# Optimization experiments

Measured on AMD Instinct MI355X. Metric: run time of the kernel, lower is better.

The kernel has to match this reference:

```python
import jax, jax.numpy as jnp
import numpy as np

N = 400000   # nodes; must equal E because the original code computes `out + x` with out per-edge
E = 400000   # edges
HID = 128
HEADS = 4
NEG_SLOPE = 0.01  # torch F.leaky_relu default


def setup_inputs() -> dict:
    key = jax.random.key(0)
    k1, k2, k3, k4 = jax.random.split(key, 4)
    x = jax.random.normal(k1, (N, HID), dtype=jnp.float32)
    edge_index = jax.random.randint(k2, (2, E), 0, N, dtype=jnp.int64)
    # xavier-uniform-ish scale for the attention parameter [1, heads, 2*hidden]
    lim_a = float(np.sqrt(6.0 / (1 + HEADS * 2 * HID)))
    attention = jax.random.uniform(k3, (1, HEADS, 2 * HID), jnp.float32, -lim_a, lim_a)
    lim_w = float(np.sqrt(1.0 / (HID * HEADS)))
    W = jax.random.uniform(k4, (HID, HID * HEADS), jnp.float32, -lim_w, lim_w)
    b = jnp.zeros((HID,), jnp.float32)
    return {"x": x, "edge_index": edge_index, "attention": attention, "W": W, "b": b}


def _scatter_softmax(s, seg, num_segments):
    # softmax over edges grouped by destination node index `seg` (axis 0)
    m = jax.lax.stop_gradient(jax.ops.segment_max(s, seg, num_segments=num_segments))
    ex = jnp.exp(s - m[seg])
    denom = jax.ops.segment_sum(ex, seg, num_segments=num_segments)
    return ex / denom[seg]


def reference(x, edge_index, attention, W, b):
    row, col = edge_index[0], edge_index[1]
    # [E, 2*HID] per-edge concatenated features
    ef = jnp.concatenate([x[row], x[col]], axis=-1)
    # per-head scores: (ef[:,None,:] * attention).sum(-1) -> [E, HEADS]
    scores = jnp.einsum('ef,hf->eh', ef, attention[0])
    scores = jax.nn.leaky_relu(scores, NEG_SLOPE)
    scores = jax.nn.softmax(scores, axis=1)      # softmax across heads (as in source)
    # dropout(p=0.1) -> identity in eval mode
    alpha = _scatter_softmax(scores, row, N)     # [E, HEADS] per-destination softmax
    # per-head weighted source features, concatenated over heads -> [E, HEADS*HID]
    feats = (alpha[:, :, None] * x[col][:, None, :]).reshape(E, HEADS * HID)
    out = feats @ W.T + b                        # Linear(hidden*heads -> hidden)
    return out + x
```

## Files before the change

kernel.cpp:

```cpp
#include <hip/hip_runtime.h>

#define NN 400000
#define NE 400000

typedef __attribute__((ext_vector_type(4))) float f32x4;
typedef __attribute__((ext_vector_type(8))) short s16x8;
typedef unsigned short ushort_t;

__device__ __forceinline__ ushort_t f2bf(float f) {
    union { float f; unsigned int u; } c;
    c.f = f;
    unsigned int u = c.u;
    u = u + 0x7fffu + ((u >> 16) & 1u);
    return (ushort_t)(u >> 16);
}
__device__ __forceinline__ float bf2f(ushort_t v) {
    union { unsigned int u; float f; } c;
    c.u = ((unsigned int)v) << 16;
    return c.f;
}

__global__ void k_detect(const int* __restrict__ ei_raw, int* __restrict__ flag) {
    if (threadIdx.x == 0 && blockIdx.x == 0) {
        int is64 = 1;
        for (int i = 0; i < 64; i++)
            if (ei_raw[2 * i + 1] != 0) { is64 = 0; break; }
        flag[0] = is64;
    }
}

__global__ void k_cvt_idx(const int* __restrict__ ei_raw, const int* __restrict__ flag,
                          int* __restrict__ ei32) {
    const int i = blockIdx.x * 256 + threadIdx.x;
    const int f = flag[0];
    ei32[i] = f ? ei_raw[2 * i] : ei_raw[i];
}

__global__ void k_wcvt(const float* __restrict__ W, ushort_t* __restrict__ wbf) {
    const int i = blockIdx.x * 256 + threadIdx.x;
    wbf[i] = f2bf(W[i]);
}

__global__ void k_uv_cvt(const float* __restrict__ x, const float* __restrict__ att,
                         ushort_t* __restrict__ xbf, float* __restrict__ uv) {
    const int lane = threadIdx.x & 63;
    const int wid = threadIdx.x >> 6;
    const int g = lane & 15;
    const int ns = lane >> 4;

    float areg[8][8];
#pragma unroll
    for (int h = 0; h < 4; h++) {
        const f32x4 fa = *(const f32x4*)(att + h * 256 + g * 8);
        const f32x4 fb = *(const f32x4*)(att + h * 256 + g * 8 + 4);
        const f32x4 ba = *(const f32x4*)(att + h * 256 + 128 + g * 8);
        const f32x4 bb = *(const f32x4*)(att + h * 256 + 128 + g * 8 + 4);
#pragma unroll
        for (int m = 0; m < 4; m++) {
            areg[h][m] = fa[m];     areg[h][4 + m] = fb[m];
            areg[4 + h][m] = ba[m]; areg[4 + h][4 + m] = bb[m];
        }
    }

    for (int tile = blockIdx.x; tile < NN / 32; tile += gridDim.x) {
        const int nb = tile * 32 + wid * 8 + ns;
#pragma unroll
        for (int t = 0; t < 2; t++) {
            const int n = nb + t * 4;
            const f32x4 xa = *(const f32x4*)(x + (size_t)n * 128 + g * 8);
            const f32x4 xb = *(const f32x4*)(x + (size_t)n * 128 + g * 8 + 4);
            s16x8 pk;
#pragma unroll
            for (int m = 0; m < 4; m++) { pk[m] = (short)f2bf(xa[m]); pk[4 + m] = (short)f2bf(xb[m]); }
            *(s16x8*)(xbf + (size_t)n * 128 + g * 8) = pk;
            float r[8];
#pragma unroll
            for (int v = 0; v < 8; v++) {
                float s = 0.f;
#pragma unroll
                for (int m = 0; m < 4; m++) s += xa[m] * areg[v][m];
#pragma unroll
                for (int m = 0; m < 4; m++) s += xb[m] * areg[v][4 + m];
                r[v] = s;
            }
#pragma unroll
            for (int mask = 1; mask <= 4; mask <<= 1)
#pragma unroll
                for (int v = 0; v < 8; v++) r[v] += __shfl_xor(r[v], mask, 64);
            const int gv = g & 7;
            float s = r[0];
#pragma unroll
            for (int v = 1; v < 8; v++) s = (gv == v) ? r[v] : s;
            s += __shfl_xor(s, 8, 64);
            if (g < 8) uv[(size_t)n * 8 + g] = s;
        }
    }
}

__global__ void k_edge(const int* __restrict__ ei, const float* __restrict__ uv,
                       float* __restrict__ p, float* __restrict__ denom) {
    const int e = blockIdx.x * 256 + threadIdx.x;
    if (e >= NE) return;
    const int row = ei[e];
    const int col = ei[NE + e];
    const f32x4 u = *(const f32x4*)(uv + (size_t)row * 8);
    const f32x4 v = *(const f32x4*)(uv + (size_t)col * 8 + 4);
    float s[4];
    float mx = -1e30f;
#pragma unroll
    for (int h = 0; h < 4; h++) {
        float t = u[h] + v[h];
        t = t > 0.f ? t : 0.01f * t;
        s[h] = t;
        mx = fmaxf(mx, t);
    }
    float ex[4], sum = 0.f;
#pragma unroll
    for (int h = 0; h < 4; h++) { ex[h] = __expf(s[h] - mx); sum += ex[h]; }
    const float inv = 1.f / sum;
    f32x4 pv;
#pragma unroll
    for (int h = 0; h < 4; h++) pv[h] = __expf(ex[h] * inv);
    *(f32x4*)(p + (size_t)e * 4) = pv;
#pragma unroll
    for (int h = 0; h < 4; h++) atomicAdd(denom + (size_t)row * 4 + h, pv[h]);
}

__global__ __launch_bounds__(256) void k_gemm(
    const ushort_t* __restrict__ xbf, const int* __restrict__ ei,
    const float* __restrict__ p, const float* __restrict__ denom,
    const ushort_t* __restrict__ wbf, const float* __restrict__ bias,
    float* __restrict__ out)
{
    __shared__ __align__(16) ushort_t Asm[128 * 128];
    __shared__ __align__(16) float alp_s[4][128];

    const int tid = threadIdx.x;
    const int lane = tid & 63;
    const int w = tid >> 6;
    const int e0 = blockIdx.x * 128;

    {
        const int e_loc = tid >> 1, half = tid & 1;
        const int col = ei[NE + e0 + e_loc];
        const ushort_t* src = xbf + (size_t)col * 128 + half * 64;
#pragma unroll
        for (int q = 0; q < 8; q++) {
            const s16x8 v = *(const s16x8*)(src + q * 8);
            const int byte = e_loc * 256 + ((half * 128 + q * 16) ^ ((e_loc & 15) << 4));
            *(s16x8*)((char*)Asm + byte) = v;
        }
    }
    if (tid < 128) {
        const int e = e0 + tid;
        const int row = ei[e];
        const f32x4 pv = *(const f32x4*)(p + (size_t)e * 4);
        const f32x4 dv = *(const f32x4*)(denom + (size_t)row * 4);
#pragma unroll
        for (int h = 0; h < 4; h++) alp_s[h][tid] = pv[h] / dv[h];
    }
    s16x8 bfr[4][4][2];
#pragma unroll
    for (int cb = 0; cb < 2; cb++) {
        const ushort_t* bbase = wbf + (size_t)(w * 32 + cb * 16 + (lane & 15)) * 512 + (lane >> 4) * 8;
#pragma unroll
        for (int h = 0; h < 4; h++)
#pragma unroll
            for (int ks = 0; ks < 4; ks++)
                bfr[h][ks][cb] = *(const s16x8*)(bbase + h * 128 + ks * 32);
    }
    float bias_r[2];
#pragma unroll
    for (int cb = 0; cb < 2; cb++) bias_r[cb] = bias[w * 32 + cb * 16 + (lane & 15)];

    __syncthreads();

    const f32x4 zero = {0.f, 0.f, 0.f, 0.f};

#pragma unroll 1
    for (int t = 0; t < 4; t++) {
        s16x8 af[2][4];
#pragma unroll
        for (int eb = 0; eb < 2; eb++) {
            const int rr = t * 32 + eb * 16 + (lane & 15);
#pragma unroll
            for (int ks = 0; ks < 4; ks++) {
                const int byte = rr * 256 + ((ks * 64 + (lane >> 4) * 16) ^ ((rr & 15) << 4));
                af[eb][ks] = *(const s16x8*)((const char*)Asm + byte);
            }
        }
        f32x4 fin[2][2];
#pragma unroll
        for (int eb = 0; eb < 2; eb++)
#pragma unroll
            for (int cb = 0; cb < 2; cb++) fin[eb][cb] = zero;

#pragma unroll
        for (int h = 0; h < 4; h++) {
            f32x4 av[2];
#pragma unroll
            for (int eb = 0; eb < 2; eb++)
                av[eb] = *(const f32x4*)&alp_s[h][t * 32 + eb * 16 + (lane >> 4) * 4];
#pragma unroll
            for (int eb = 0; eb < 2; eb++)
#pragma unroll
                for (int cb = 0; cb < 2; cb++) {
                    f32x4 a = __builtin_amdgcn_mfma_f32_16x16x32_bf16(af[eb][0], bfr[h][0][cb], zero, 0, 0, 0);
#pragma unroll
                    for (int ks = 1; ks < 4; ks++)
                        a = __builtin_amdgcn_mfma_f32_16x16x32_bf16(af[eb][ks], bfr[h][ks][cb], a, 0, 0, 0);
                    fin[eb][cb] += av[eb] * a;
                }
        }
#pragma unroll
        for (int eb = 0; eb < 2; eb++)
#pragma unroll
            for (int cb = 0; cb < 2; cb++) {
                const int i = w * 32 + cb * 16 + (lane & 15);
#pragma unroll
                for (int r = 0; r < 4; r++) {
                    const int e = e0 + t * 32 + eb * 16 + (lane >> 4) * 4 + r;
                    const size_t off = (size_t)e * 128 + i;
                    out[off] = fin[eb][cb][r] + bias_r[cb] + bf2f(xbf[off]);
                }
            }
    }
}

extern "C" void kernel_launch(void* const* d_in, const int* in_sizes, int n_in,
                              void* d_out, int out_size, void* d_ws, size_t ws_size,
                              hipStream_t stream) {
    const float* x      = (const float*)d_in[0];
    const int*   ei_raw = (const int*)d_in[1];
    const float* att    = (const float*)d_in[2];
    const float* W      = (const float*)d_in[3];
    const float* b      = (const float*)d_in[4];
    float* out = (float*)d_out;

    char* ws = (char*)d_ws;
    float*    uv      = (float*)(ws);
    float*    p       = (float*)(ws + 12800000);
    float*    denom   = (float*)(ws + 19200000);
    ushort_t* wbf     = (ushort_t*)(ws + 32000000);
    int*      flag    = (int*)(ws + 32200000);
    int*      ei32    = (int*)(ws + 32200064);
    ushort_t* xbf     = (ushort_t*)(ws + 35400192);

    hipMemsetAsync(denom, 0, (size_t)NN * 4 * sizeof(float), stream);
    k_detect<<<1, 64, 0, stream>>>(ei_raw, flag);
    k_cvt_idx<<<2 * NE / 256, 256, 0, stream>>>(ei_raw, flag, ei32);
    k_wcvt<<<256, 256, 0, stream>>>(W, wbf);
    k_uv_cvt<<<2048, 256, 0, stream>>>(x, att, xbf, uv);
    k_edge<<<(NE + 255) / 256, 256, 0, stream>>>(ei32, uv, p, denom);
    k_gemm<<<NE / 128, 256, 0, stream>>>(xbf, ei32, p, denom, wbf, b, out);
}
```

Measured before the change: 302.1 us.

## Restructure GEMM so each wave owns 32 edges and streams W from cache

Each wave now handles its own 32 edges across all 128 output columns. The gathered x[col] rows are loaded straight into MFMA A-fragment registers, so the shared-memory staging and the __syncthreads are gone. Attention weights are spread across lanes with shuffles instead of an LDS array. W fragments are reloaded per column block from global/L2 instead of being held in registers, which cuts register pressure and allows a min-blocks launch bound of 4 for higher occupancy. The cost is more W reads from cache and less coalesced per-lane gathers.

Result: slower. 414.6 us (+37.3%).

```diff
diff --git a/kernel.cpp b/kernel.cpp
--- a/kernel.cpp
+++ b/kernel.cpp
@@ -126,104 +126,84 @@
     for (int h = 0; h < 4; h++) atomicAdd(denom + (size_t)row * 4 + h, pv[h]);
 }
 
-__global__ __launch_bounds__(256) void k_gemm(
+__global__ __launch_bounds__(256, 4) void k_gemm(
     const ushort_t* __restrict__ xbf, const int* __restrict__ ei,
     const float* __restrict__ p, const float* __restrict__ denom,
     const ushort_t* __restrict__ wbf, const float* __restrict__ bias,
     float* __restrict__ out)
 {
-    __shared__ __align__(16) ushort_t Asm[128 * 128];
-    __shared__ __align__(16) float alp_s[4][128];
-
     const int tid = threadIdx.x;
     const int lane = tid & 63;
     const int w = tid >> 6;
-    const int e0 = blockIdx.x * 128;
-
+    const int et = blockIdx.x * 128 + w * 32;
+
+    int colr[2];
+#pragma unroll
+    for (int eb = 0; eb < 2; eb++)
+        colr[eb] = ei[NE + et + eb * 16 + (lane & 15)];
+    s16x8 af[2][4];
+#pragma unroll
+    for (int eb = 0; eb < 2; eb++) {
+        const ushort_t* src = xbf + (size_t)colr[eb] * 128 + (lane >> 4) * 8;
+#pragma unroll
+        for (int ks = 0; ks < 4; ks++)
+            af[eb][ks] = *(const s16x8*)(src + ks * 32);
+    }
+
+    f32x4 alp;
     {
-        const int e_loc = tid >> 1, half = tid & 1;
-        const int col = ei[NE + e0 + e_loc];
-        const ushort_t* src = xbf + (size_t)col * 128 + half * 64;
-#pragma unroll
-        for (int q = 0; q < 8; q++) {
-            const s16x8 v = *(const s16x8*)(src + q * 8);
-            const int byte = e_loc * 256 + ((half * 128 + q * 16) ^ ((e_loc & 15) << 4));
-            *(s16x8*)((char*)Asm + byte) = v;
-        }
-    }
-    if (tid < 128) {
-        const int e = e0 + tid;
+        const int e = et + (lane & 31);
         const int row = ei[e];
         const f32x4 pv = *(const f32x4*)(p + (size_t)e * 4);
         const f32x4 dv = *(const f32x4*)(denom + (size_t)row * 4);
-#pragma unroll
-        for (int h = 0; h < 4; h++) alp_s[h][tid] = pv[h] / dv[h];
-    }
-    s16x8 bfr[4][4][2];
-#pragma unroll
-    for (int cb = 0; cb < 2; cb++) {
-        const ushort_t* bbase = wbf + (size_t)(w * 32 + cb * 16 + (lane & 15)) * 512 + (lane >> 4) * 8;
-#pragma unroll
-        for (int h = 0; h < 4; h++)
+        alp = pv / dv;
+    }
+    f32x4 av[4][2];
+#pragma unroll
+    for (int h = 0; h < 4; h++)
+#pragma unroll
+        for (int eb = 0; eb < 2; eb++)
+#pragma unroll
+            for (int r = 0; r < 4; r++)
+                av[h][eb][r] = __shfl(alp[h], eb * 16 + (lane >> 4) * 4 + r, 64);
+
+    const f32x4 zero = {0.f, 0.f, 0.f, 0.f};
+
+#pragma unroll 1
+    for (int cb = 0; cb < 8; cb++) {
+        const int icol = cb * 16 + (lane & 15);
+        const ushort_t* bbase = wbf + (size_t)icol * 512 + (lane >> 4) * 8;
+        f32x4 fin0 = zero, fin1 = zero;
+#pragma unroll
+        for (int h = 0; h < 4; h++) {
+            s16x8 bfr[4];
 #pragma unroll
             for (int ks = 0; ks < 4; ks++)
-                bfr[h][ks][cb] = *(const s16x8*)(bbase + h * 128 + ks * 32);
-    }
-    float bias_r[2];
-#pragma unroll
-    for (int cb = 0; cb < 2; cb++) bias_r[cb] = bias[w * 32 + cb * 16 + (lane & 15)];
-
-    __syncthreads();
-
-    const f32x4 zero = {0.f, 0.f, 0.f, 0.f};
-
-#pragma unroll 1
-    for (int t = 0; t < 4; t++) {
-        s16x8 af[2][4];
-#pragma unroll
-        for (int eb = 0; eb < 2; eb++) {
-            const int rr = t * 32 + eb * 16 + (lane & 15);
-#pragma unroll
-            for (int ks = 0; ks < 4; ks++) {
-                const int byte = rr * 256 + ((ks * 64 + (lane >> 4) * 16) ^ ((rr & 15) << 4));
-                af[eb][ks] = *(const s16x8*)((const char*)Asm + byte);
-            }
-        }
-        f32x4 fin[2][2];
-#pragma unroll
-        for (int eb = 0; eb < 2; eb++)
-#pragma unroll
-            for (int cb = 0; cb < 2; cb++) fin[eb][cb] = zero;
-
-#pragma unroll
-        for (int h = 0; h < 4; h++) {
-            f32x4 av[2];
-#pragma unroll
-            for (int eb = 0; eb < 2; eb++)
-                av[eb] = *(const f32x4*)&alp_s[h][t * 32 + eb * 16 + (lane >> 4) * 4];
-#pragma unroll
-            for (int eb = 0; eb < 2; eb++)
-#pragma unroll
-                for (int cb = 0; cb < 2; cb++) {
-                    f32x4 a = __builtin_amdgcn_mfma_f32_16x16x32_bf16(af[eb][0], bfr[h][0][cb], zero, 0, 0, 0);
-#pragma unroll
-                    for (int ks = 1; ks < 4; ks++)
-                        a = __builtin_amdgcn_mfma_f32_16x16x32_bf16(af[eb][ks], bfr[h][ks][cb], a, 0, 0, 0);
-                    fin[eb][cb] += av[eb] * a;
-                }
-        }
-#pragma unroll
-        for (int eb = 0; eb < 2; eb++)
-#pragma unroll
-            for (int cb = 0; cb < 2; cb++) {
-                const int i = w * 32 + cb * 16 + (lane & 15);
-#pragma unroll
-                for (int r = 0; r < 4; r++) {
-                    const int e = e0 + t * 32 + eb * 16 + (lane >> 4) * 4 + r;
-                    const size_t off = (size_t)e * 128 + i;
-                    out[off] = fin[eb][cb][r] + bias_r[cb] + bf2f(xbf[off]);
-                }
-            }
+                bfr[ks] = *(const s16x8*)(bbase + h * 128 + ks * 32);
+            f32x4 a0 = __builtin_amdgcn_mfma_f32_16x16x32_bf16(af[0][0], bfr[0], zero, 0, 0, 0);
+            f32x4 a1 = __builtin_amdgcn_mfma_f32_16x16x32_bf16(af[1][0], bfr[0], zero, 0, 0, 0);
+#pragma unroll
+            for (int ks = 1; ks < 4; ks++) {
+                a0 = __builtin_amdgcn_mfma_f32_16x16x32_bf16(af[0][ks], bfr[ks], a0, 0, 0, 0);
+                a1 = __builtin_amdgcn_mfma_f32_16x16x32_bf16(af[1][ks], bfr[ks], a1, 0, 0, 0);
+            }
+            fin0 += av[h][0] * a0;
+            fin1 += av[h][1] * a1;
+        }
+        const float bias_r = bias[icol];
+#pragma unroll
+        for (int r = 0; r < 4; r++) {
+            {
+                const int e = et + (lane >> 4) * 4 + r;
+                const size_t off = (size_t)e * 128 + icol;
+                out[off] = fin0[r] + bias_r + bf2f(xbf[off]);
+            }
+            {
+                const int e = et + 16 + (lane >> 4) * 4 + r;
+                const size_t off = (size_t)e * 128 + icol;
+                out[off] = fin1[r] + bias_r + bf2f(xbf[off]);
+            }
+        }
     }
 }
 
```
